# Performance work log

Measured on AMD Instinct MI355X. Metric: run time of the kernel, lower is better.

Reference implementation:

```python
import jax, jax.numpy as jnp
import numpy as np

H = 12          # num_attention_heads
DH = 64         # attention_head_size
EPS = 1e-12     # F.normalize eps
MAX_LOG_SCALE = float(np.log(1.0 / 0.01))  # clamp max for logit_scale


def _l2norm(x):
    # F.normalize(x, dim=-1): x / max(||x||_2, eps)
    n = jnp.sqrt(jnp.sum(x * x, axis=-1, keepdims=True))
    return x / jnp.maximum(n, EPS)


def setup_inputs() -> dict:
    key = jax.random.key(0)
    ks = jax.random.split(key, 9)
    B, S, D = 4, 2048, 768
    sd = 1.0 / np.sqrt(D)
    inp = {
        "hidden_states": jax.random.normal(ks[0], (B, S, D), jnp.float32),
        "Wq": jax.random.normal(ks[1], (D, D), jnp.float32) * sd,
        "bq": jnp.zeros((D,), jnp.float32),
        "Wk": jax.random.normal(ks[2], (D, D), jnp.float32) * sd,
        "bk": jnp.zeros((D,), jnp.float32),
        "Wv": jax.random.normal(ks[3], (D, D), jnp.float32) * sd,
        "bv": jnp.zeros((D,), jnp.float32),
        "Wo": jax.random.normal(ks[4], (D, D), jnp.float32) * sd,
        "bo": jnp.zeros((D,), jnp.float32),
        "logit_scale": jnp.log(10.0 * jnp.ones((H, 1, 1), jnp.float32)),
    }
    return inp


def reference(hidden_states, Wq, bq, Wk, bk, Wv, bv, Wo, bo, logit_scale):
    B, S, D = hidden_states.shape
    # QKV projections (torch Linear: x @ W.T + b), split heads -> [B,H,S,DH]
    def proj(W, b):
        y = hidden_states @ W.T + b
        return y.reshape(B, S, H, DH).transpose(0, 2, 1, 3)
    q = proj(Wq, bq)
    k = proj(Wk, bk)
    v = proj(Wv, bv)
    # cosine-similarity scores scaled by clamped-exp per-head logit scale
    scale = jnp.exp(jnp.minimum(logit_scale, MAX_LOG_SCALE))  # [H,1,1]
    scores = jnp.einsum('bhqd,bhkd->bhqk', _l2norm(q), _l2norm(k)) * scale[None]
    probs = jax.nn.softmax(scores, axis=-1)
    ctx = jnp.einsum('bhqk,bhkd->bhqd', probs, v)
    ctx = ctx.transpose(0, 2, 1, 3).reshape(B, S, D)
    return ctx @ Wo.T + bo
```

## Files before the change

### kernel.cpp

```cpp
#include <hip/hip_runtime.h>
#include <math.h>

#define Hh 12
#define S_LEN 2048
#define D_MODEL 768
#define HD 64

static constexpr float MAXLS = 4.6051701859880914f;

typedef short bf16x8 __attribute__((ext_vector_type(8)));
typedef float f32x4  __attribute__((ext_vector_type(4)));
typedef float f32x16 __attribute__((ext_vector_type(16)));
typedef unsigned short u16x4 __attribute__((ext_vector_type(4)));
typedef unsigned short u16x8 __attribute__((ext_vector_type(8)));
typedef unsigned int u32x4 __attribute__((ext_vector_type(4)));

__device__ __forceinline__ unsigned short f2bf(float x) {
    unsigned int u = __builtin_bit_cast(unsigned int, x);
    unsigned int r = (u + 0x7FFF + ((u >> 16) & 1)) >> 16;
    return (unsigned short)r;
}

__device__ __forceinline__ unsigned int cvtpk(float a, float b) {
    unsigned int r;
    asm("v_cvt_pk_bf16_f32 %0, %1, %2" : "=v"(r) : "v"(a), "v"(b));
    return r;
}

__device__ __forceinline__ void gload16(const void* g, void* l) {
    __builtin_amdgcn_global_load_lds(
        (const __attribute__((address_space(1))) unsigned int*)g,
        (__attribute__((address_space(3))) unsigned int*)l, 16, 0, 0);
}

__global__ __launch_bounds__(256)
void convert_bf16(const float* __restrict__ hs,
                  const float* __restrict__ Wq, const float* __restrict__ Wk,
                  const float* __restrict__ Wv, const float* __restrict__ Wo,
                  unsigned short* __restrict__ hsb,
                  unsigned short* __restrict__ wqkvb,
                  unsigned short* __restrict__ wob)
{
    const long long N0 = 8192LL * 768;
    const long long NW = 768LL * 768;
    const long long e  = ((long long)blockIdx.x * 256 + threadIdx.x) * 8;
    const float* src; unsigned short* dst;
    if (e < N0) { src = hs + e; dst = hsb + e; }
    else if (e < N0 + 3*NW) {
        const long long r = e - N0;
        const int z = (int)(r / NW);
        src = (z == 0 ? Wq : z == 1 ? Wk : Wv) + (r - (long long)z * NW);
        dst = wqkvb + r;
    } else {
        const long long r = e - N0 - 3*NW;
        src = Wo + r; dst = wob + r;
    }
    const float4 f0 = *(const float4*)src;
    const float4 f1 = *(const float4*)(src + 4);
    u16x8 o;
    o[0]=f2bf(f0.x); o[1]=f2bf(f0.y); o[2]=f2bf(f0.z); o[3]=f2bf(f0.w);
    o[4]=f2bf(f1.x); o[5]=f2bf(f1.y); o[6]=f2bf(f1.z); o[7]=f2bf(f1.w);
    *(u16x8*)dst = o;
}

template<int MODE>
__global__ __launch_bounds__(256)
void gemm_bf16(const unsigned short* __restrict__ A,
               const unsigned short* __restrict__ Wt,
               const float* __restrict__ b0, const float* __restrict__ b1,
               const float* __restrict__ b2, const float* __restrict__ ls,
               unsigned short* __restrict__ qb, unsigned short* __restrict__ kb,
               unsigned short* __restrict__ vt, float* __restrict__ out)
{
    constexpr int K = 768;
    __shared__ char As[16384];
    __shared__ char Bs[16384];

    const int tid = threadIdx.x, w = tid >> 6, l = tid & 63;
    const int wr = w >> 1, wc = w & 1, hi = l >> 4, ll = l & 15;
    const int n0 = blockIdx.x * 128, m0 = blockIdx.y * 128;

    const int srow = l >> 3;
    const int sch  = (l & 7) ^ srow;
    const char* Ab = (const char*)(A  + (size_t)(m0 + w*32) * K) + srow * (K*2) + sch * 16;
    const char* Bb = (const char*)(Wt + (size_t)(n0 + w*32) * K) + srow * (K*2) + sch * 16;
    char* AsW = As + (w*32) * 128;
    char* BsW = Bs + (w*32) * 128;

    f32x4 acc[4][4];
    #pragma unroll
    for (int i = 0; i < 4; ++i)
        #pragma unroll
        for (int j = 0; j < 4; ++j) acc[i][j] = (f32x4){0.f,0.f,0.f,0.f};

    for (int kt = 0; kt < K/64; ++kt) {
        __syncthreads();
        #pragma unroll
        for (int s = 0; s < 4; ++s) {
            gload16(Ab + kt*128 + s*8*(K*2), AsW + s*1024);
            gload16(Bb + kt*128 + s*8*(K*2), BsW + s*1024);
        }
        __syncthreads();

        bf16x8 af[2][4], bf[2][4];
        #pragma unroll
        for (int kk = 0; kk < 2; ++kk) {
            const int pc = kk*4 + hi;
            #pragma unroll
            for (int i = 0; i < 4; ++i) {
                const int ra = wr*64 + i*16 + ll;
                af[kk][i] = *(const bf16x8*)(As + ra*128 + ((pc ^ (ra & 7)) << 4));
                const int rb = wc*64 + i*16 + ll;
                bf[kk][i] = *(const bf16x8*)(Bs + rb*128 + ((pc ^ (rb & 7)) << 4));
            }
        }
        #pragma unroll
        for (int kk = 0; kk < 2; ++kk)
            #pragma unroll
            for (int i = 0; i < 4; ++i)
                #pragma unroll
                for (int j = 0; j < 4; ++j)
                    acc[i][j] = __builtin_amdgcn_mfma_f32_16x16x32_bf16(af[kk][i], bf[kk][j], acc[i][j], 0, 0, 0);
    }

    if (MODE == 0) {
        const int z  = n0 / 768;
        const int nl = (n0 % 768) + wc*64;
        const int h  = nl >> 6;
        const int b  = m0 >> 11;
        const int s0 = (m0 & (S_LEN-1)) + wr*64;
        const float* bias = (z == 0) ? b0 : (z == 1) ? b1 : b2;
        float bj[4];
        #pragma unroll
        for (int j = 0; j < 4; ++j) bj[j] = bias[nl + j*16 + ll];

        if (z < 2) {
            const float sc = (z == 0) ? expf(fminf(ls[h], MAXLS)) : 1.0f;
            unsigned short* dst = (z == 0 ? qb : kb) + ((size_t)(b*Hh + h) * S_LEN) * HD;
            #pragma unroll
            for (int i = 0; i < 4; ++i) {
                #pragma unroll
                for (int r = 0; r < 4; ++r) {
                    float v[4]; float ss = 0.f;
                    #pragma unroll
                    for (int j = 0; j < 4; ++j) { v[j] = acc[i][j][r] + bj[j]; ss += v[j]*v[j]; }
                    #pragma unroll
                    for (int mm = 1; mm < 16; mm <<= 1) ss += __shfl_xor(ss, mm, 64);
                    const float inv = sc / fmaxf(sqrtf(ss), 1e-12f);
                    const int s = s0 + i*16 + hi*4 + r;
                    #pragma unroll
                    for (int j = 0; j < 4; ++j)
                        dst[(size_t)s * HD + j*16 + ll] = f2bf(v[j] * inv);
                }
            }
        } else {
            const int hsw = ((hi & 1) << 1) | (hi >> 1);
            #pragma unroll
            for (int j = 0; j < 4; ++j) {
                const int d = (nl & 63) + j*16 + ll;
                #pragma unroll
                for (int i = 0; i < 4; ++i) {
                    const int s = s0 + i*16 + hsw*4;
                    u16x4 o;
                    #pragma unroll
                    for (int r = 0; r < 4; ++r) o[r] = f2bf(acc[i][j][r] + bj[j]);
                    *(u16x4*)(vt + ((size_t)(b*Hh + h) * HD + d) * S_LEN + s) = o;
                }
            }
        }
    } else {
        #pragma unroll
        for (int i = 0; i < 4; ++i)
            #pragma unroll
            for (int j = 0; j < 4; ++j) {
                const int n = n0 + wc*64 + j*16 + ll;
                const float bn = b0[n];
                #pragma unroll
                for (int r = 0; r < 4; ++r) {
                    const int m = m0 + wr*64 + i*16 + hi*4 + r;
                    out[(size_t)m * D_MODEL + n] = acc[i][j][r] + bn;
                }
            }
    }
}

__global__ __launch_bounds__(256)
void attn_mfma2(const char* __restrict__ qb_, const char* __restrict__ kb_,
                const char* __restrict__ vtb_, const float* __restrict__ ls,
                unsigned short* __restrict__ ctx)
{
    __shared__ char smem[16384];
    char* Ks = smem;
    char* Vs = smem + 8192;

    const int flat = blockIdx.x;
    const int xcd = flat & 7, ix = flat >> 3;
    const int bh = xcd * 6 + (ix >> 4);
    const int q0 = (ix & 15) * 128;
    const int b = bh / Hh, h = bh % Hh;

    const int tid = threadIdx.x, w = tid >> 6, l = tid & 63;
    const int lq = l & 31, g = l >> 5;

    const float c1 = 1.4426950408889634f;
    const float sc = __expf(fminf(ls[h], MAXLS));
    const float c0 = -sc * c1;

    const char* qg = qb_ + ((size_t)bh * S_LEN + q0 + w * 32) * 128;
    const char* kg = kb_ + (size_t)bh * S_LEN * 128;
    const char* vg = vtb_ + (size_t)bh * HD * (S_LEN * 2);

    bf16x8 qf[4];
    #pragma unroll
    for (int s = 0; s < 4; ++s)
        qf[s] = *(const bf16x8*)(qg + lq * 128 + s * 32 + g * 16);

    f32x16 acco0, acco1;
    #pragma unroll
    for (int i = 0; i < 16; ++i) { acco0[i] = 0.f; acco1[i] = 0.f; }
    float lsum = 0.f;

    const int srow = l >> 3;
    const int schb = ((l & 7) ^ srow) << 4;
    const char* kst = kg + (size_t)(w * 16 + srow) * 128 + schb;
    const char* vst = vg + (size_t)(w * 16 + srow) * 4096 + schb;
    char* kld = Ks + (w * 16) * 128;
    char* vld = Vs + (w * 16) * 128;
    const int swzq = (lq & 7);

    for (int kt = 0; kt < S_LEN / 64; ++kt) {
        __syncthreads();
        gload16(kst + kt * 8192, kld);
        gload16(kst + kt * 8192 + 8 * 128, kld + 1024);
        gload16(vst + kt * 128, vld);
        gload16(vst + kt * 128 + (size_t)8 * 4096, vld + 1024);
        __syncthreads();

        f32x16 sa0, sa1;
        #pragma unroll
        for (int i = 0; i < 16; ++i) { sa0[i] = 0.f; sa1[i] = 0.f; }

        __builtin_amdgcn_s_setprio(1);
        #pragma unroll
        for (int s = 0; s < 4; ++s) {
            const int c = 2 * s + g;
            const bf16x8 kf0 = *(const bf16x8*)(Ks + lq * 128 + ((c ^ swzq) << 4));
            sa0 = __builtin_amdgcn_mfma_f32_32x32x16_bf16(kf0, qf[s], sa0, 0, 0, 0);
            const bf16x8 kf1 = *(const bf16x8*)(Ks + (32 + lq) * 128 + ((c ^ swzq) << 4));
            sa1 = __builtin_amdgcn_mfma_f32_32x32x16_bf16(kf1, qf[s], sa1, 0, 0, 0);
        }
        __builtin_amdgcn_s_setprio(0);

        unsigned int pw[2][8];
        #pragma unroll
        for (int n = 0; n < 2; ++n) {
            const f32x16 sv = n ? sa1 : sa0;
            #pragma unroll
            for (int m = 0; m < 4; ++m) {
                const float p0 = __builtin_amdgcn_exp2f(fmaf(sv[4*m+0], c1, c0));
                const float p1 = __builtin_amdgcn_exp2f(fmaf(sv[4*m+1], c1, c0));
                const float p2 = __builtin_amdgcn_exp2f(fmaf(sv[4*m+2], c1, c0));
                const float p3 = __builtin_amdgcn_exp2f(fmaf(sv[4*m+3], c1, c0));
                lsum += (p0 + p1) + (p2 + p3);
                pw[n][2*m]   = cvtpk(p0, p1);
                pw[n][2*m+1] = cvtpk(p2, p3);
            }
        }

        __builtin_amdgcn_s_setprio(1);
        #pragma unroll
        for (int t = 0; t < 4; ++t) {
            u32x4 pu;
            pu[0] = pw[t>>1][4*(t&1)+0];
            pu[1] = pw[t>>1][4*(t&1)+1];
            pu[2] = pw[t>>1][4*(t&1)+2];
            pu[3] = pw[t>>1][4*(t&1)+3];
            const bf16x8 pa = __builtin_bit_cast(bf16x8, pu);
            const int c = 2 * t + g;
            const bf16x8 vf0 = *(const bf16x8*)(Vs + lq * 128 + ((c ^ swzq) << 4));
            acco0 = __builtin_amdgcn_mfma_f32_32x32x16_bf16(pa, vf0, acco0, 0, 0, 0);
            const bf16x8 vf1 = *(const bf16x8*)(Vs + (32 + lq) * 128 + ((c ^ swzq) << 4));
            acco1 = __builtin_amdgcn_mfma_f32_32x32x16_bf16(pa, vf1, acco1, 0, 0, 0);
        }
        __builtin_amdgcn_s_setprio(0);
    }

    lsum += __shfl_xor(lsum, 32, 64);
    #pragma unroll
    for (int r = 0; r < 16; ++r) {
        const int qrow = (r & 3) + 8 * (r >> 2) + 4 * g;
        const float inv = 1.0f / __shfl(lsum, (l & 32) | qrow, 64);
        unsigned short* crow = ctx + ((size_t)b * S_LEN + q0 + w * 32 + qrow) * D_MODEL + h * HD;
        crow[lq]      = f2bf(acco0[r] * inv);
        crow[32 + lq] = f2bf(acco1[r] * inv);
    }
}

extern "C" void kernel_launch(void* const* d_in, const int* in_sizes, int n_in,
                              void* d_out, int out_size, void* d_ws, size_t ws_size,
                              hipStream_t stream)
{
    const float* hs = (const float*)d_in[0];
    const float* Wq = (const float*)d_in[1];
    const float* bq = (const float*)d_in[2];
    const float* Wk = (const float*)d_in[3];
    const float* bk = (const float*)d_in[4];
    const float* Wv = (const float*)d_in[5];
    const float* bv = (const float*)d_in[6];
    const float* Wo = (const float*)d_in[7];
    const float* bo = (const float*)d_in[8];
    const float* ls = (const float*)d_in[9];
    float* out = (float*)d_out;

    const int B = 4;
    const size_t nHS = 8192ULL * 768;
    const size_t nW  = 768ULL * 768;
    const size_t nPB = (size_t)B * Hh * S_LEN * HD;

    unsigned short* hsb   = (unsigned short*)d_ws;
    unsigned short* wqkvb = hsb + nHS;
    unsigned short* wob   = wqkvb + 3 * nW;
    unsigned short* qbuf  = wob + nW;
    unsigned short* kbuf  = qbuf + nPB;
    unsigned short* vtb   = kbuf + nPB;
    unsigned short* cbuf  = vtb + nPB;

    hipLaunchKernelGGL(convert_bf16, dim3(4224), dim3(256), 0, stream,
                       hs, Wq, Wk, Wv, Wo, hsb, wqkvb, wob);

    hipLaunchKernelGGL((gemm_bf16<0>), dim3(2304/128, 8192/128), dim3(256), 0, stream,
                       hsb, wqkvb, bq, bk, bv, ls, qbuf, kbuf, vtb, nullptr);

    hipLaunchKernelGGL(attn_mfma2, dim3((S_LEN/128) * B * Hh), dim3(256), 0, stream,
                       (const char*)qbuf, (const char*)kbuf, (const char*)vtb, ls, cbuf);

    hipLaunchKernelGGL((gemm_bf16<1>), dim3(768/128, 8192/128), dim3(256), 0, stream,
                       cbuf, wob, bo, nullptr, nullptr, nullptr,
                       nullptr, nullptr, nullptr, out);
}
```

Baseline: 241.1 us.

## Double-buffer K/V tiles in attention and use chunk-major LDS layout

The attention kernel now double-buffers its K and V tiles in 32KB of LDS. It issues the global-to-LDS loads for the next key tile before computing on the current one, and keeps a single barrier per iteration instead of two. The LDS layout also changes from row-major with an XOR swizzle to a chunk-major layout, where each lane loads one key row's 16-byte chunk, so MFMA operand reads become contiguous. The intent is to overlap memory latency with MFMA work. The cost is double the LDS per block, which may reduce occupancy, and the new layout may change bank-conflict and global-coalescing behaviour.

```diff
diff --git a/kernel.cpp b/kernel.cpp
--- a/kernel.cpp
+++ b/kernel.cpp
@@ -185,13 +185,11 @@
 }
 
 __global__ __launch_bounds__(256)
-void attn_mfma2(const char* __restrict__ qb_, const char* __restrict__ kb_,
+void attn_mfma3(const char* __restrict__ qb_, const char* __restrict__ kb_,
                 const char* __restrict__ vtb_, const float* __restrict__ ls,
                 unsigned short* __restrict__ ctx)
 {
-    __shared__ char smem[16384];
-    char* Ks = smem;
-    char* Vs = smem + 8192;
+    __shared__ char smem[32768];
 
     const int flat = blockIdx.x;
     const int xcd = flat & 7, ix = flat >> 3;
@@ -207,8 +205,8 @@
     const float c0 = -sc * c1;
 
     const char* qg = qb_ + ((size_t)bh * S_LEN + q0 + w * 32) * 128;
-    const char* kg = kb_ + (size_t)bh * S_LEN * 128;
-    const char* vg = vtb_ + (size_t)bh * HD * (S_LEN * 2);
+    const char* kg = kb_ + (size_t)bh * S_LEN * 128 + (size_t)l * 128;
+    const char* vg = vtb_ + (size_t)bh * HD * (S_LEN * 2) + (size_t)l * 4096;
 
     bf16x8 qf[4];
     #pragma unroll
@@ -220,21 +218,23 @@
     for (int i = 0; i < 16; ++i) { acco0[i] = 0.f; acco1[i] = 0.f; }
     float lsum = 0.f;
 
-    const int srow = l >> 3;
-    const int schb = ((l & 7) ^ srow) << 4;
-    const char* kst = kg + (size_t)(w * 16 + srow) * 128 + schb;
-    const char* vst = vg + (size_t)(w * 16 + srow) * 4096 + schb;
-    char* kld = Ks + (w * 16) * 128;
-    char* vld = Vs + (w * 16) * 128;
-    const int swzq = (lq & 7);
+#define STAGE(buf, kt) do {                                                  \
+        char* dstS = smem + ((buf) << 14);                                   \
+        gload16(kg + (size_t)(kt) * 8192 + w * 16,        dstS + w * 1024);          \
+        gload16(kg + (size_t)(kt) * 8192 + (w+4) * 16,    dstS + (w+4) * 1024);      \
+        gload16(vg + (size_t)(kt) * 128 + w * 16,         dstS + 8192 + w * 1024);   \
+        gload16(vg + (size_t)(kt) * 128 + (w+4) * 16,     dstS + 8192 + (w+4) * 1024); \
+    } while (0)
+
+    STAGE(0, 0);
+    __syncthreads();
+    int cur = 0;
 
     for (int kt = 0; kt < S_LEN / 64; ++kt) {
-        __syncthreads();
-        gload16(kst + kt * 8192, kld);
-        gload16(kst + kt * 8192 + 8 * 128, kld + 1024);
-        gload16(vst + kt * 128, vld);
-        gload16(vst + kt * 128 + (size_t)8 * 4096, vld + 1024);
-        __syncthreads();
+        if (kt < S_LEN / 64 - 1) STAGE(cur ^ 1, kt + 1);
+
+        const char* Ks = smem + (cur << 14);
+        const char* Vs = Ks + 8192;
 
         f32x16 sa0, sa1;
         #pragma unroll
@@ -243,10 +243,9 @@
         __builtin_amdgcn_s_setprio(1);
         #pragma unroll
         for (int s = 0; s < 4; ++s) {
-            const int c = 2 * s + g;
-            const bf16x8 kf0 = *(const bf16x8*)(Ks + lq * 128 + ((c ^ swzq) << 4));
+            const bf16x8 kf0 = *(const bf16x8*)(Ks + (2*s + g) * 1024 + lq * 16);
             sa0 = __builtin_amdgcn_mfma_f32_32x32x16_bf16(kf0, qf[s], sa0, 0, 0, 0);
-            const bf16x8 kf1 = *(const bf16x8*)(Ks + (32 + lq) * 128 + ((c ^ swzq) << 4));
+            const bf16x8 kf1 = *(const bf16x8*)(Ks + (2*s + g) * 1024 + 512 + lq * 16);
             sa1 = __builtin_amdgcn_mfma_f32_32x32x16_bf16(kf1, qf[s], sa1, 0, 0, 0);
         }
         __builtin_amdgcn_s_setprio(0);
@@ -276,14 +275,17 @@
             pu[2] = pw[t>>1][4*(t&1)+2];
             pu[3] = pw[t>>1][4*(t&1)+3];
             const bf16x8 pa = __builtin_bit_cast(bf16x8, pu);
-            const int c = 2 * t + g;
-            const bf16x8 vf0 = *(const bf16x8*)(Vs + lq * 128 + ((c ^ swzq) << 4));
+            const bf16x8 vf0 = *(const bf16x8*)(Vs + (2*t + g) * 1024 + lq * 16);
             acco0 = __builtin_amdgcn_mfma_f32_32x32x16_bf16(pa, vf0, acco0, 0, 0, 0);
-            const bf16x8 vf1 = *(const bf16x8*)(Vs + (32 + lq) * 128 + ((c ^ swzq) << 4));
+            const bf16x8 vf1 = *(const bf16x8*)(Vs + (2*t + g) * 1024 + 512 + lq * 16);
             acco1 = __builtin_amdgcn_mfma_f32_32x32x16_bf16(pa, vf1, acco1, 0, 0, 0);
         }
         __builtin_amdgcn_s_setprio(0);
-    }
+
+        __syncthreads();
+        cur ^= 1;
+    }
+#undef STAGE
 
     lsum += __shfl_xor(lsum, 32, 64);
     #pragma unroll
@@ -331,7 +333,7 @@
     hipLaunchKernelGGL((gemm_bf16<0>), dim3(2304/128, 8192/128), dim3(256), 0, stream,
                        hsb, wqkvb, bq, bk, bv, ls, qbuf, kbuf, vtb, nullptr);
 
-    hipLaunchKernelGGL(attn_mfma2, dim3((S_LEN/128) * B * Hh), dim3(256), 0, stream,
+    hipLaunchKernelGGL(attn_mfma3, dim3((S_LEN/128) * B * Hh), dim3(256), 0, stream,
                        (const char*)qbuf, (const char*)kbuf, (const char*)vtb, ls, cbuf);
 
     hipLaunchKernelGGL((gemm_bf16<1>), dim3(768/128, 8192/128), dim3(256), 0, stream,
```

Measured after the change: 241.3 us. No clear change (+0.1%).
